# Kernel tuning notes

Hardware: AMD Instinct MI355X
Metric: run time of the kernel (lower is better)

The kernel has to match this reference:

```python
import jax, jax.numpy as jnp
import numpy as np

EPS = 1e-5  # torch InstanceNorm1d default


def _instance_norm_lastdim(t):
    # torch InstanceNorm1d applied to (b*h, n, d): normalizes over last axis d
    # per (b, h, n) with biased variance, no affine.
    mu = jnp.mean(t, axis=-1, keepdims=True)
    var = jnp.var(t, axis=-1, keepdims=True)
    return (t - mu) * jax.lax.rsqrt(var + EPS)


def setup_inputs() -> dict:
    key = jax.random.key(0)
    k1, k2, k3, k4 = jax.random.split(key, 4)
    b, n, dim = 4, 8192, 128
    heads, dim_head = 8, 64
    inner = heads * dim_head
    x = jax.random.normal(k1, (b, n, dim), dtype=jnp.float32)
    # nn.Linear(dim, inner*3, bias=False): weight (out, in); we store transposed (in, out)
    w_qkv = jax.random.normal(k2, (dim, inner * 3), dtype=jnp.float32) * (1.0 / np.sqrt(dim))
    w_out = jax.random.normal(k3, (inner, dim), dtype=jnp.float32) * (1.0 / np.sqrt(inner))
    b_out = jax.random.normal(k4, (dim,), dtype=jnp.float32) * 0.01
    return {"x": x, "w_qkv": w_qkv, "w_out": w_out, "b_out": b_out}


def reference(x, w_qkv, w_out, b_out):
    b, n, _ = x.shape
    heads, dim_head = 8, 64
    qkv = x @ w_qkv  # (b, n, 3*inner)
    q, k, v = jnp.split(qkv, 3, axis=-1)

    def to_heads(t):
        return t.reshape(b, n, heads, dim_head).transpose(0, 2, 1, 3)  # b h n d

    q, k, v = to_heads(q), to_heads(k), to_heads(v)
    # galerkin: norm k and v (InstanceNorm over dim_head axis)
    k = _instance_norm_lastdim(k)
    v = _instance_norm_lastdim(v)
    dots = jnp.einsum('bhnd,bhne->bhde', k, v)      # K^T V, small (d x d)
    out = jnp.einsum('bhnd,bhde->bhne', q, dots) * (1.0 / n)
    out = out.transpose(0, 2, 1, 3).reshape(b, n, heads * dim_head)
    return out @ w_out + b_out
```

## Files before the change

kernel.cpp:

```cpp
#include <hip/hip_runtime.h>

#define NN 8192
#define DIM 128

typedef short short8 __attribute__((ext_vector_type(8)));
typedef float f32x4 __attribute__((ext_vector_type(4)));

__device__ __forceinline__ unsigned short f2bf(float f) {
  unsigned int u = __float_as_uint(f);
  u = (u + 0x7FFFu + ((u >> 16) & 1u)) >> 16;
  return (unsigned short)u;
}
__device__ __forceinline__ unsigned int cvtpk(float a, float b) {
  unsigned int r;
  asm("v_cvt_pk_bf16_f32 %0, %1, %2" : "=v"(r) : "v"(a), "v"(b));
  return r;
}
__device__ __forceinline__ void gll16(const void* gsrc, void* ldst) {
  __builtin_amdgcn_global_load_lds(
      (const __attribute__((address_space(1))) unsigned int*)gsrc,
      (__attribute__((address_space(3))) unsigned int*)ldst, 16, 0, 0);
}
#define BAR_LGKM()                                          \
  do {                                                      \
    asm volatile("s_waitcnt lgkmcnt(0)" ::: "memory");      \
    __builtin_amdgcn_sched_barrier(0);                      \
    __builtin_amdgcn_s_barrier();                           \
    __builtin_amdgcn_sched_barrier(0);                      \
  } while (0)
#define BAR_VM()                                            \
  do {                                                      \
    asm volatile("s_waitcnt vmcnt(0)" ::: "memory");        \
    __builtin_amdgcn_sched_barrier(0);                      \
    __builtin_amdgcn_s_barrier();                           \
    __builtin_amdgcn_sched_barrier(0);                      \
  } while (0)

__global__ __launch_bounds__(256) void prep_kernel(const float* __restrict__ x,
                                                   const float* __restrict__ wqkv,
                                                   unsigned char* __restrict__ ximg,
                                                   unsigned char* __restrict__ wimg,
                                                   float* __restrict__ dots) {
  __shared__ __align__(16) unsigned char wb[32768];
  const int t = threadIdx.x;
  const int bx = blockIdx.x;
  if (bx < 1024) {
#pragma unroll
    for (int rep = 0; rep < 2; ++rep) {
      const int idx = bx * 512 + rep * 256 + t;
      const int bt = idx >> 10;
      const int o = (idx & 1023) << 4;
      const int r = o >> 8;
      const int q0 = o & 255;
      const int c0 = (q0 ^ ((r & 7) << 4)) >> 1;
      const float* src = x + ((size_t)(bt >> 7) * NN + (size_t)(bt & 127) * 64 + r) * DIM + c0;
      const float4 v0 = *(const float4*)src;
      const float4 v1 = *(const float4*)(src + 4);
      uint4 u;
      u.x = cvtpk(v0.x, v0.y);
      u.y = cvtpk(v0.z, v0.w);
      u.z = cvtpk(v1.x, v1.y);
      u.w = cvtpk(v1.z, v1.w);
      *(uint4*)(ximg + (size_t)idx * 16) = u;
    }
  } else if (bx < 1032) {
    const int h = bx - 1024;
    const int k = t >> 1;
    const int chalf = t & 1;
    const float* wp = wqkv + (size_t)k * 1536 + (chalf ? (1024 + h * 64) : (512 + h * 64));
    const float4* wp4 = (const float4*)wp;
    const int c0 = chalf * 64;
    float4 wv[16];
    float sum = 0.f;
#pragma unroll
    for (int jj = 0; jj < 16; ++jj) {
      wv[jj] = wp4[jj];
      sum += wv[jj].x + wv[jj].y + wv[jj].z + wv[jj].w;
    }
    const float mean = sum * (1.f / 64.f);
#pragma unroll
    for (int jj = 0; jj < 16; ++jj) {
      const int c = c0 + jj * 4;
      const unsigned int cx0 = (unsigned int)((c + 0) & 7) << 4;
      const unsigned int cx1 = (unsigned int)((c + 1) & 7) << 4;
      const unsigned int cx2 = (unsigned int)((c + 2) & 7) << 4;
      const unsigned int cx3 = (unsigned int)((c + 3) & 7) << 4;
      *(unsigned short*)(wb + (c + 0) * 256 + (((unsigned)(2 * k)) ^ cx0)) = f2bf(wv[jj].x - mean);
      *(unsigned short*)(wb + (c + 1) * 256 + (((unsigned)(2 * k)) ^ cx1)) = f2bf(wv[jj].y - mean);
      *(unsigned short*)(wb + (c + 2) * 256 + (((unsigned)(2 * k)) ^ cx2)) = f2bf(wv[jj].z - mean);
      *(unsigned short*)(wb + (c + 3) * 256 + (((unsigned)(2 * k)) ^ cx3)) = f2bf(wv[jj].w - mean);
    }
    __syncthreads();
    const uint4* s4 = (const uint4*)(wb + t * 128);
    uint4* d4 = (uint4*)(wimg + (size_t)h * 32768 + t * 128);
#pragma unroll
    for (int i = 0; i < 8; ++i) d4[i] = s4[i];
  } else {
    const int zb = bx - 1032;
    float4* dz = (float4*)dots + (size_t)zb * 4096 + t;
    const float4 z = make_float4(0.f, 0.f, 0.f, 0.f);
#pragma unroll
    for (int i = 0; i < 16; ++i) dz[i * 256] = z;
  }
}

__global__ __launch_bounds__(256) void kv_dots_v2(const unsigned char* __restrict__ ximg,
                                                  const unsigned char* __restrict__ wimg,
                                                  float* __restrict__ dots) {
  __shared__ __align__(16) unsigned char smem[81920];
  unsigned char* const XB0 = smem;
  unsigned char* const XB1 = smem + 16384;
  unsigned char* const WB = smem + 32768;
  unsigned char* const KT = smem + 65536;
  unsigned char* const VT = smem + 73728;

  const int t = threadIdx.x;
  const int bx = blockIdx.x;
  const int h = bx >> 7;
  const int p = bx & 127;
  const int b = p >> 5;
  const int chunk = p & 31;

  const int wave = t >> 6;
  const int lane = t & 63;
  const int lb = lane & 15;
  const int kg = lane >> 4;
  const unsigned int lxor = (unsigned int)(lb & 7) << 4;

  const unsigned char* wsrc = wimg + (size_t)h * 32768;
  const unsigned char* xsrc = ximg + (size_t)(b * 128 + chunk * 4) * 16384;

#pragma unroll
  for (int i = 0; i < 8; ++i)
    gll16(wsrc + (wave * 8 + i) * 1024 + lane * 16, WB + (wave * 8 + i) * 1024);
#pragma unroll
  for (int i = 0; i < 4; ++i)
    gll16(xsrc + (wave * 4 + i) * 1024 + lane * 16, XB0 + (wave * 4 + i) * 1024);

  f32x4 dacc[4];
#pragma unroll
  for (int nt = 0; nt < 4; ++nt) dacc[nt] = (f32x4)0.f;

  BAR_VM();

  unsigned char* XBc = XB0;
  unsigned char* XBn = XB1;
  const int arow = wave * 16 + lb;

  for (int tile = 0; tile < 4; ++tile) {
    if (tile < 3) {
#pragma unroll
      for (int i = 0; i < 4; ++i)
        gll16(xsrc + (size_t)(tile + 1) * 16384 + (wave * 4 + i) * 1024 + lane * 16,
              XBn + (wave * 4 + i) * 1024);
    }

    f32x4 acc[8];
#pragma unroll
    for (int ct = 0; ct < 8; ++ct) acc[ct] = (f32x4)0.f;
#pragma unroll
    for (int ks = 0; ks < 4; ++ks) {
      const unsigned int koff = (unsigned int)(ks * 64 + kg * 16);
      const short8 a = *(const short8*)(XBc + arow * 256 + (koff ^ lxor));
#pragma unroll
      for (int ct = 0; ct < 8; ++ct) {
        const short8 bf = *(const short8*)(WB + (ct * 16 + lb) * 256 + (koff ^ lxor));
        acc[ct] = __builtin_amdgcn_mfma_f32_16x16x32_bf16(a, bf, acc[ct], 0, 0, 0);
      }
    }

    float kscale[4];
#pragma unroll
    for (int e = 0; e < 4; ++e) {
      float sk = acc[0][e] * acc[0][e] + acc[1][e] * acc[1][e] +
                 acc[2][e] * acc[2][e] + acc[3][e] * acc[3][e];
      float sv = acc[4][e] * acc[4][e] + acc[5][e] * acc[5][e] +
                 acc[6][e] * acc[6][e] + acc[7][e] * acc[7][e];
      sk += __shfl_xor(sk, 1); sv += __shfl_xor(sv, 1);
      sk += __shfl_xor(sk, 2); sv += __shfl_xor(sv, 2);
      sk += __shfl_xor(sk, 4); sv += __shfl_xor(sv, 4);
      sk += __shfl_xor(sk, 8); sv += __shfl_xor(sv, 8);
      kscale[e] = rsqrtf(sk * (1.f / 64.f) + 1e-5f) * rsqrtf(sv * (1.f / 64.f) + 1e-5f);
    }

    {
      const unsigned int rb2 = (unsigned int)(32 * wave + kg * 8);
#pragma unroll
      for (int ct = 0; ct < 4; ++ct) {
        uint2 w;
        w.x = cvtpk(acc[ct][0] * kscale[0], acc[ct][1] * kscale[1]);
        w.y = cvtpk(acc[ct][2] * kscale[2], acc[ct][3] * kscale[3]);
        *(uint2*)(KT + (ct * 16 + lb) * 128 + (rb2 ^ lxor)) = w;
      }
#pragma unroll
      for (int ct = 4; ct < 8; ++ct) {
        uint2 w;
        w.x = cvtpk(acc[ct][0], acc[ct][1]);
        w.y = cvtpk(acc[ct][2], acc[ct][3]);
        *(uint2*)(VT + ((ct - 4) * 16 + lb) * 128 + (rb2 ^ lxor)) = w;
      }
    }
    BAR_LGKM();

#pragma unroll
    for (int ks2 = 0; ks2 < 2; ++ks2) {
      const unsigned int koff = (unsigned int)(ks2 * 64 + kg * 16);
      const short8 a = *(const short8*)(KT + (wave * 16 + lb) * 128 + (koff ^ lxor));
#pragma unroll
      for (int nt = 0; nt < 4; ++nt) {
        const short8 bf = *(const short8*)(VT + (nt * 16 + lb) * 128 + (koff ^ lxor));
        dacc[nt] = __builtin_amdgcn_mfma_f32_16x16x32_bf16(a, bf, dacc[nt], 0, 0, 0);
      }
    }
    BAR_VM();

    unsigned char* tmp = XBc; XBc = XBn; XBn = tmp;
  }

  float* dp = dots + (size_t)(b * 8 + h) * 4096;
#pragma unroll
  for (int nt = 0; nt < 4; ++nt) {
#pragma unroll
    for (int reg = 0; reg < 4; ++reg) {
      const int d = 16 * wave + kg * 4 + reg;
      const int e = nt * 16 + lb;
      atomicAdd(&dp[d * 64 + e], dacc[nt][reg]);
    }
  }
}

template <int TR>
__global__ __launch_bounds__(256) void tw_kernel(const float* __restrict__ wqkv,
                                                 const float* __restrict__ wout,
                                                 const float* __restrict__ dots,
                                                 float* __restrict__ part) {
  __shared__ __align__(16) float ds[64 * 66];
  __shared__ __align__(16) float wqT[64 * 36];
  __shared__ __align__(16) float Ts[32 * 66];
  __shared__ __align__(16) float wos[64 * 132];

  const int blk = blockIdx.x;
  const int bh = blk >> 2;
  const int cq = blk & 3;
  const int h = bh & 7;
  const int t = threadIdx.x;

  for (int i = t; i < 4096; i += 256)
    ds[(i >> 6) * 66 + (i & 63)] = dots[(size_t)bh * 4096 + i];

  for (int i = t; i < 2048; i += 256) {
    const int d = i >> 5;
    const int c = i & 31;
    wqT[d * 36 + c] = wqkv[(size_t)(cq * 32 + c) * 1536 + h * 64 + d];
  }

  for (int i = t; i < 2048; i += 256) {
    const int e = i >> 5;
    const int jj = (i & 31) * 4;
    *(float4*)&wos[e * 132 + jj] = *(const float4*)(wout + (size_t)(h * 64 + e) * 128 + jj);
  }
  __syncthreads();

  {
    const int c = t >> 3;
    const int e0 = (t & 7) * 8;
    float acc[8];
#pragma unroll
    for (int q = 0; q < 8; ++q) acc[q] = 0.f;
    for (int d = 0; d < 64; ++d) {
      const float wq = wqT[d * 36 + c];
      const float4 d0 = *(const float4*)&ds[d * 66 + e0];
      const float4 d1 = *(const float4*)&ds[d * 66 + e0 + 4];
      acc[0] += wq * d0.x; acc[1] += wq * d0.y; acc[2] += wq * d0.z; acc[3] += wq * d0.w;
      acc[4] += wq * d1.x; acc[5] += wq * d1.y; acc[6] += wq * d1.z; acc[7] += wq * d1.w;
    }
    *(float4*)&Ts[c * 66 + e0] = make_float4(acc[0], acc[1], acc[2], acc[3]);
    *(float4*)&Ts[c * 66 + e0 + 4] = make_float4(acc[4], acc[5], acc[6], acc[7]);
  }
  __syncthreads();

  {
    const int c = t >> 3;
    const int j0 = (t & 7) * 16;
    float acc[16];
#pragma unroll
    for (int q = 0; q < 16; ++q) acc[q] = 0.f;
    for (int e = 0; e < 64; ++e) {
      const float tv = Ts[c * 66 + e];
#pragma unroll
      for (int q = 0; q < 16; q += 4) {
        const float4 wv = *(const float4*)&wos[e * 132 + j0 + q];
        acc[q + 0] += tv * wv.x;
        acc[q + 1] += tv * wv.y;
        acc[q + 2] += tv * wv.z;
        acc[q + 3] += tv * wv.w;
      }
    }
    if (TR) {
      float* pp = part + (size_t)bh * 16384;
      const int cc = cq * 32 + c;
#pragma unroll
      for (int q = 0; q < 16; ++q) pp[(j0 + q) * 128 + cc] = acc[q];
    } else {
      float* pp = part + (size_t)bh * 16384 + (size_t)(cq * 32 + c) * 128 + j0;
#pragma unroll
      for (int q = 0; q < 16; q += 4)
        *(float4*)&pp[q] = make_float4(acc[q], acc[q + 1], acc[q + 2], acc[q + 3]);
    }
  }
}

__global__ __launch_bounds__(256) void bigw_reduce_v2(const float* __restrict__ part,
                                                      unsigned char* __restrict__ bigwimg) {
  const int idx = blockIdx.x * 256 + threadIdx.x;
  const int b = idx >> 11;
  const int o = (idx & 2047) << 4;
  const int j = o >> 8;
  const int q0 = o & 255;
  const int c0 = (q0 ^ ((j & 7) << 4)) >> 1;
  float s[8];
#pragma unroll
  for (int i = 0; i < 8; ++i) s[i] = 0.f;
  const float* pb = part + (size_t)b * 8 * 16384 + j * 128 + c0;
#pragma unroll
  for (int hh = 0; hh < 8; ++hh) {
    const float4 p0 = *(const float4*)(pb + hh * 16384);
    const float4 p1 = *(const float4*)(pb + hh * 16384 + 4);
    s[0] += p0.x; s[1] += p0.y; s[2] += p0.z; s[3] += p0.w;
    s[4] += p1.x; s[5] += p1.y; s[6] += p1.z; s[7] += p1.w;
  }
  const float inv_n = 1.f / (float)NN;
  uint4 u;
  u.x = cvtpk(s[0] * inv_n, s[1] * inv_n);
  u.y = cvtpk(s[2] * inv_n, s[3] * inv_n);
  u.z = cvtpk(s[4] * inv_n, s[5] * inv_n);
  u.w = cvtpk(s[6] * inv_n, s[7] * inv_n);
  *(uint4*)(bigwimg + (size_t)idx * 16) = u;
}

__global__ __launch_bounds__(256) void out_v2(const unsigned char* __restrict__ ximg,
                                              const unsigned char* __restrict__ bigwimg,
                                              const float* __restrict__ bout,
                                              float* __restrict__ out) {
  __shared__ __align__(16) unsigned char smem[49152];
  unsigned char* const XB = smem;
  unsigned char* const WJ = smem + 16384;

  const int t = threadIdx.x;
  const int bx = blockIdx.x;
  const int b = bx >> 7;
  const int tile = bx & 127;

  const int wave = t >> 6;
  const int lane = t & 63;
  const int lb = lane & 15;
  const int kg = lane >> 4;
  const unsigned int lxor = (unsigned int)(lb & 7) << 4;

  const unsigned char* wsrc = bigwimg + (size_t)b * 32768;
  const unsigned char* xsrc = ximg + (size_t)(b * 128 + tile) * 16384;

#pragma unroll
  for (int i = 0; i < 8; ++i)
    gll16(wsrc + (wave * 8 + i) * 1024 + lane * 16, WJ + (wave * 8 + i) * 1024);
#pragma unroll
  for (int i = 0; i < 4; ++i)
    gll16(xsrc + (wave * 4 + i) * 1024 + lane * 16, XB + (wave * 4 + i) * 1024);

  float bias[8];
#pragma unroll
  for (int ct = 0; ct < 8; ++ct) bias[ct] = bout[ct * 16 + lb];

  BAR_VM();

  f32x4 acc[8];
#pragma unroll
  for (int ct = 0; ct < 8; ++ct) acc[ct] = (f32x4)0.f;
  const int arow = wave * 16 + lb;
#pragma unroll
  for (int ks = 0; ks < 4; ++ks) {
    const unsigned int koff = (unsigned int)(ks * 64 + kg * 16);
    const short8 a = *(const short8*)(XB + arow * 256 + (koff ^ lxor));
#pragma unroll
    for (int ct = 0; ct < 8; ++ct) {
      const short8 bf = *(const short8*)(WJ + (ct * 16 + lb) * 256 + (koff ^ lxor));
      acc[ct] = __builtin_amdgcn_mfma_f32_16x16x32_bf16(a, bf, acc[ct], 0, 0, 0);
    }
  }

  float* op = out + (size_t)(b * NN + tile * 64 + 16 * wave + kg * 4) * DIM;
#pragma unroll
  for (int ct = 0; ct < 8; ++ct) {
#pragma unroll
    for (int reg = 0; reg < 4; ++reg) {
      op[reg * DIM + ct * 16 + lb] = acc[ct][reg] + bias[ct];
    }
  }
}

__global__ __launch_bounds__(256) void zero_dots_fb(float* __restrict__ dots) {
  float4* dz = (float4*)dots + (size_t)blockIdx.x * 4096 + threadIdx.x;
  const float4 z = make_float4(0.f, 0.f, 0.f, 0.f);
#pragma unroll
  for (int i = 0; i < 16; ++i) dz[i * 256] = z;
}

__global__ __launch_bounds__(256) void kv_dots_fb(const float* __restrict__ x,
                                                  const float* __restrict__ wqkv,
                                                  float* __restrict__ dots) {
  __shared__ __align__(16) unsigned char smem[49152];
  unsigned char* const XB = smem;
  unsigned char* const KT = smem;
  unsigned char* const VT = smem + 8192;
  unsigned char* const WB = smem + 16384;

  const int t = threadIdx.x;
  const int bx = blockIdx.x;
  const int h = bx >> 7;
  const int p = bx & 127;
  const int b = p >> 5;
  const int chunk = p & 31;
  const int row0 = chunk * 256;

  const int wave = t >> 6;
  const int lane = t & 63;
  const int lb = lane & 15;
  const int kg = lane >> 4;
  const unsigned int lxor = (unsigned int)(lb & 7) << 4;

  {
    const int k = t >> 1;
    const int chalf = t & 1;
    const float* wp = wqkv + (size_t)k * 1536 + (chalf ? (1024 + h * 64) : (512 + h * 64));
    const float4* wp4 = (const float4*)wp;
    const int c0 = chalf * 64;
    float4 wv[16];
    float sum = 0.f;
#pragma unroll
    for (int jj = 0; jj < 16; ++jj) {
      wv[jj] = wp4[jj];
      sum += wv[jj].x + wv[jj].y + wv[jj].z + wv[jj].w;
    }
    const float mean = sum * (1.f / 64.f);
#pragma unroll
    for (int jj = 0; jj < 16; ++jj) {
      const int c = c0 + jj * 4;
      const unsigned int cx0 = (unsigned int)((c + 0) & 7) << 4;
      const unsigned int cx1 = (unsigned int)((c + 1) & 7) << 4;
      const unsigned int cx2 = (unsigned int)((c + 2) & 7) << 4;
      const unsigned int cx3 = (unsigned int)((c + 3) & 7) << 4;
      *(unsigned short*)(WB + (c + 0) * 256 + (((unsigned)(2 * k)) ^ cx0)) = f2bf(wv[jj].x - mean);
      *(unsigned short*)(WB + (c + 1) * 256 + (((unsigned)(2 * k)) ^ cx1)) = f2bf(wv[jj].y - mean);
      *(unsigned short*)(WB + (c + 2) * 256 + (((unsigned)(2 * k)) ^ cx2)) = f2bf(wv[jj].z - mean);
      *(unsigned short*)(WB + (c + 3) * 256 + (((unsigned)(2 * k)) ^ cx3)) = f2bf(wv[jj].w - mean);
    }
  }

  f32x4 dacc[4];
#pragma unroll
  for (int nt = 0; nt < 4; ++nt) dacc[nt] = (f32x4)0.f;

  __syncthreads();

  for (int tile = 0; tile < 4; ++tile) {
    const int rowbase = row0 + tile * 64;
    __syncthreads();
    {
      const int r = t >> 2;
      const int cb = (t & 3) * 32;
      const float4* gp4 = (const float4*)(x + (size_t)(b * NN + rowbase + r) * DIM + cb);
      const unsigned int rxor = (unsigned int)(r & 7) << 4;
#pragma unroll
      for (int jj = 0; jj < 4; ++jj) {
        const float4 v0 = gp4[2 * jj];
        const float4 v1 = gp4[2 * jj + 1];
        uint4 u;
        u.x = cvtpk(v0.x, v0.y);
        u.y = cvtpk(v0.z, v0.w);
        u.z = cvtpk(v1.x, v1.y);
        u.w = cvtpk(v1.z, v1.w);
        *(uint4*)(XB + r * 256 + (((unsigned)(2 * cb + 16 * jj)) ^ rxor)) = u;
      }
    }
    __syncthreads();

    f32x4 acc[8];
#pragma unroll
    for (int ct = 0; ct < 8; ++ct) acc[ct] = (f32x4)0.f;
    const int arow = wave * 16 + lb;
#pragma unroll
    for (int ks = 0; ks < 4; ++ks) {
      const unsigned int koff = (unsigned int)(ks * 64 + kg * 16);
      const short8 a = *(const short8*)(XB + arow * 256 + (koff ^ lxor));
#pragma unroll
      for (int ct = 0; ct < 8; ++ct) {
        const short8 bf = *(const short8*)(WB + (ct * 16 + lb) * 256 + (koff ^ lxor));
        acc[ct] = __builtin_amdgcn_mfma_f32_16x16x32_bf16(a, bf, acc[ct], 0, 0, 0);
      }
    }

    float kscale[4];
#pragma unroll
    for (int e = 0; e < 4; ++e) {
      float sk = acc[0][e] * acc[0][e] + acc[1][e] * acc[1][e] +
                 acc[2][e] * acc[2][e] + acc[3][e] * acc[3][e];
      float sv = acc[4][e] * acc[4][e] + acc[5][e] * acc[5][e] +
                 acc[6][e] * acc[6][e] + acc[7][e] * acc[7][e];
      sk += __shfl_xor(sk, 1); sv += __shfl_xor(sv, 1);
      sk += __shfl_xor(sk, 2); sv += __shfl_xor(sv, 2);
      sk += __shfl_xor(sk, 4); sv += __shfl_xor(sv, 4);
      sk += __shfl_xor(sk, 8); sv += __shfl_xor(sv, 8);
      kscale[e] = rsqrtf(sk * (1.f / 64.f) + 1e-5f) * rsqrtf(sv * (1.f / 64.f) + 1e-5f);
    }

    __syncthreads();
    {
      const unsigned int rb2 = (unsigned int)(32 * wave + kg * 8);
#pragma unroll
      for (int ct = 0; ct < 4; ++ct) {
        uint2 w;
        w.x = cvtpk(acc[ct][0] * kscale[0], acc[ct][1] * kscale[1]);
        w.y = cvtpk(acc[ct][2] * kscale[2], acc[ct][3] * kscale[3]);
        *(uint2*)(KT + (ct * 16 + lb) * 128 + (rb2 ^ lxor)) = w;
      }
#pragma unroll
      for (int ct = 4; ct < 8; ++ct) {
        uint2 w;
        w.x = cvtpk(acc[ct][0], acc[ct][1]);
        w.y = cvtpk(acc[ct][2], acc[ct][3]);
        *(uint2*)(VT + ((ct - 4) * 16 + lb) * 128 + (rb2 ^ lxor)) = w;
      }
    }
    __syncthreads();

#pragma unroll
    for (int ks2 = 0; ks2 < 2; ++ks2) {
      const unsigned int koff = (unsigned int)(ks2 * 64 + kg * 16);
      const short8 a = *(const short8*)(KT + (wave * 16 + lb) * 128 + (koff ^ lxor));
#pragma unroll
      for (int nt = 0; nt < 4; ++nt) {
        const short8 bf = *(const short8*)(VT + (nt * 16 + lb) * 128 + (koff ^ lxor));
        dacc[nt] = __builtin_amdgcn_mfma_f32_16x16x32_bf16(a, bf, dacc[nt], 0, 0, 0);
      }
    }
  }

  float* dp = dots + (size_t)(b * 8 + h) * 4096;
#pragma unroll
  for (int nt = 0; nt < 4; ++nt) {
#pragma unroll
    for (int reg = 0; reg < 4; ++reg) {
      const int d = 16 * wave + kg * 4 + reg;
      const int e = nt * 16 + lb;
      atomicAdd(&dp[d * 64 + e], dacc[nt][reg]);
    }
  }
}

__global__ __launch_bounds__(256) void bigw_reduce_fb(const float* __restrict__ part,
                                                      float* __restrict__ bigw) {
  const int i = blockIdx.x * 256 + threadIdx.x;
  const int b = i >> 14;
  const int cj = i & 16383;
  const float* pp = part + (size_t)b * 8 * 16384 + cj;
  float s = 0.f;
#pragma unroll
  for (int h = 0; h < 8; ++h) s += pp[h * 16384];
  bigw[i] = s * (1.f / (float)NN);
}

__global__ __launch_bounds__(256) void out_fb(const float* __restrict__ x,
                                              const float* __restrict__ bigw,
                                              const float* __restrict__ bout,
                                              float* __restrict__ out) {
  __shared__ __align__(16) unsigned char smem[49152];
  unsigned char* const XB = smem;
  unsigned char* const WB = smem + 16384;

  const int t = threadIdx.x;
  const int bx = blockIdx.x;
  const int b = bx >> 7;
  const int rowbase = (bx & 127) * 64;

  const int wave = t >> 6;
  const int lane = t & 63;
  const int lb = lane & 15;
  const int kg = lane >> 4;
  const unsigned int lxor = (unsigned int)(lb & 7) << 4;

  {
    const int c = t >> 1;
    const int jhalf = t & 1;
    const float4* wp4 = (const float4*)(bigw + (size_t)b * 16384 + (size_t)c * 128 + jhalf * 64);
    const int j0 = jhalf * 64;
#pragma unroll
    for (int q = 0; q < 16; ++q) {
      const float4 v = wp4[q];
      const int j = j0 + q * 4;
      const unsigned int jx0 = (unsigned int)((j + 0) & 7) << 4;
      const unsigned int jx1 = (unsigned int)((j + 1) & 7) << 4;
      const unsigned int jx2 = (unsigned int)((j + 2) & 7) << 4;
      const unsigned int jx3 = (unsigned int)((j + 3) & 7) << 4;
      *(unsigned short*)(WB + (j + 0) * 256 + (((unsigned)(2 * c)) ^ jx0)) = f2bf(v.x);
      *(unsigned short*)(WB + (j + 1) * 256 + (((unsigned)(2 * c)) ^ jx1)) = f2bf(v.y);
      *(unsigned short*)(WB + (j + 2) * 256 + (((unsigned)(2 * c)) ^ jx2)) = f2bf(v.z);
      *(unsigned short*)(WB + (j + 3) * 256 + (((unsigned)(2 * c)) ^ jx3)) = f2bf(v.w);
    }
  }

  float bias[8];
#pragma unroll
  for (int ct = 0; ct < 8; ++ct) bias[ct] = bout[ct * 16 + lb];

  {
    const int r = t >> 2;
    const int cb = (t & 3) * 32;
    const float4* gp4 = (const float4*)(x + (size_t)(b * NN + rowbase + r) * DIM + cb);
    const unsigned int rxor = (unsigned int)(r & 7) << 4;
#pragma unroll
    for (int jj = 0; jj < 4; ++jj) {
      const float4 v0 = gp4[2 * jj];
      const float4 v1 = gp4[2 * jj + 1];
      uint4 u;
      u.x = cvtpk(v0.x, v0.y);
      u.y = cvtpk(v0.z, v0.w);
      u.z = cvtpk(v1.x, v1.y);
      u.w = cvtpk(v1.z, v1.w);
      *(uint4*)(XB + r * 256 + (((unsigned)(2 * cb + 16 * jj)) ^ rxor)) = u;
    }
  }
  __syncthreads();

  f32x4 acc[8];
#pragma unroll
  for (int ct = 0; ct < 8; ++ct) acc[ct] = (f32x4)0.f;
  const int arow = wave * 16 + lb;
#pragma unroll
  for (int ks = 0; ks < 4; ++ks) {
    const unsigned int koff = (unsigned int)(ks * 64 + kg * 16);
    const short8 a = *(const short8*)(XB + arow * 256 + (koff ^ lxor));
#pragma unroll
    for (int ct = 0; ct < 8; ++ct) {
      const short8 bf = *(const short8*)(WB + (ct * 16 + lb) * 256 + (koff ^ lxor));
      acc[ct] = __builtin_amdgcn_mfma_f32_16x16x32_bf16(a, bf, acc[ct], 0, 0, 0);
    }
  }

  float* op = out + (size_t)(b * NN + rowbase + 16 * wave + kg * 4) * DIM;
#pragma unroll
  for (int ct = 0; ct < 8; ++ct) {
#pragma unroll
    for (int reg = 0; reg < 4; ++reg) {
      op[reg * DIM + ct * 16 + lb] = acc[ct][reg] + bias[ct];
    }
  }
}

extern "C" void kernel_launch(void* const* d_in, const int* in_sizes, int n_in,
                              void* d_out, int out_size, void* d_ws, size_t ws_size,
                              hipStream_t stream) {
  (void)in_sizes; (void)n_in; (void)out_size;
  const float* x = (const float*)d_in[0];
  const float* wqkv = (const float*)d_in[1];
  const float* wout = (const float*)d_in[2];
  const float* bout = (const float*)d_in[3];
  float* out = (float*)d_out;

  const size_t NEED = 8388608ull + 262144ull + 131072ull + 524288ull + 2097152ull;
  if (ws_size >= NEED) {
    unsigned char* ximg = (unsigned char*)d_ws;
    unsigned char* wimg = ximg + 8388608;
    unsigned char* bigwimg = wimg + 262144;
    float* dots = (float*)(bigwimg + 131072);
    float* part = dots + 131072;

    hipLaunchKernelGGL(prep_kernel, dim3(1040), dim3(256), 0, stream, x, wqkv, ximg, wimg, dots);
    hipLaunchKernelGGL(kv_dots_v2, dim3(1024), dim3(256), 0, stream, ximg, wimg, dots);
    hipLaunchKernelGGL((tw_kernel<1>), dim3(128), dim3(256), 0, stream, wqkv, wout, dots, part);
    hipLaunchKernelGGL(bigw_reduce_v2, dim3(32), dim3(256), 0, stream, part, bigwimg);
    hipLaunchKernelGGL(out_v2, dim3(512), dim3(256), 0, stream, ximg, bigwimg, bout, out);
  } else {
    float* dots = (float*)d_ws;
    float* part = dots + 131072;
    float* bigw = part + 524288;
    hipLaunchKernelGGL(zero_dots_fb, dim3(8), dim3(256), 0, stream, dots);
    hipLaunchKernelGGL(kv_dots_fb, dim3(1024), dim3(256), 0, stream, x, wqkv, dots);
    hipLaunchKernelGGL((tw_kernel<0>), dim3(128), dim3(256), 0, stream, wqkv, wout, dots, part);
    hipLaunchKernelGGL(bigw_reduce_fb, dim3(256), dim3(256), 0, stream, part, bigw);
    hipLaunchKernelGGL(out_fb, dim3(512), dim3(256), 0, stream, x, bigw, bout, out);
  }
}
```

Measured before the change: 70.56 us.

## Restructure kv_dots to 512 threads with all row tiles loaded at once

Replaces the 4-iteration double-buffered loop over 64-row X tiles in the K/V projection plus KᵀV kernel with a single pass using 8 waves. Each wave loads and projects its own 32 rows at once, writes normalized K and V transposed into a per-wave LDS slab, and then each wave accumulates one 16x32 slice of the 64x64 dots across all 8 slabs. This removes the serial tile loop and its per-tile barriers, and halves the number of atomics per thread. In exchange it uses 96KB of LDS per block, which limits occupancy, and drops the overlap of loads with compute.

```diff
diff --git a/kernel.cpp b/kernel.cpp
--- a/kernel.cpp
+++ b/kernel.cpp
@@ -104,15 +104,11 @@
   }
 }
 
-__global__ __launch_bounds__(256) void kv_dots_v2(const unsigned char* __restrict__ ximg,
+__global__ __launch_bounds__(512) void kv_dots_v3(const unsigned char* __restrict__ ximg,
                                                   const unsigned char* __restrict__ wimg,
                                                   float* __restrict__ dots) {
-  __shared__ __align__(16) unsigned char smem[81920];
-  unsigned char* const XB0 = smem;
-  unsigned char* const XB1 = smem + 16384;
-  unsigned char* const WB = smem + 32768;
-  unsigned char* const KT = smem + 65536;
-  unsigned char* const VT = smem + 73728;
+  __shared__ __align__(16) unsigned char smem[98304];
+  unsigned char* const WB = smem;
 
   const int t = threadIdx.x;
   const int bx = blockIdx.x;
@@ -126,105 +122,106 @@
   const int lb = lane & 15;
   const int kg = lane >> 4;
   const unsigned int lxor = (unsigned int)(lb & 7) << 4;
-
-  const unsigned char* wsrc = wimg + (size_t)h * 32768;
-  const unsigned char* xsrc = ximg + (size_t)(b * 128 + chunk * 4) * 16384;
-
-#pragma unroll
-  for (int i = 0; i < 8; ++i)
-    gll16(wsrc + (wave * 8 + i) * 1024 + lane * 16, WB + (wave * 8 + i) * 1024);
-#pragma unroll
-  for (int i = 0; i < 4; ++i)
-    gll16(xsrc + (wave * 4 + i) * 1024 + lane * 16, XB0 + (wave * 4 + i) * 1024);
-
-  f32x4 dacc[4];
-#pragma unroll
-  for (int nt = 0; nt < 4; ++nt) dacc[nt] = (f32x4)0.f;
-
+  const unsigned int rxor2 = (unsigned int)(lb & 3) << 4;
+
+  unsigned char* const PW = smem + 32768 + wave * 8192;
+
+  {
+    const unsigned char* wsrc = wimg + (size_t)h * 32768;
+#pragma unroll
+    for (int i = 0; i < 4; ++i)
+      gll16(wsrc + (wave * 4 + i) * 1024 + lane * 16, WB + (wave * 4 + i) * 1024);
+    const unsigned char* xsrc = ximg +
+        (size_t)(b * 128 + chunk * 4 + (wave >> 1)) * 16384 + (size_t)(wave & 1) * 8192;
+#pragma unroll
+    for (int i = 0; i < 8; ++i)
+      gll16(xsrc + i * 1024 + lane * 16, PW + i * 1024);
+  }
   BAR_VM();
 
-  unsigned char* XBc = XB0;
-  unsigned char* XBn = XB1;
-  const int arow = wave * 16 + lb;
-
-  for (int tile = 0; tile < 4; ++tile) {
-    if (tile < 3) {
-#pragma unroll
-      for (int i = 0; i < 4; ++i)
-        gll16(xsrc + (size_t)(tile + 1) * 16384 + (wave * 4 + i) * 1024 + lane * 16,
-              XBn + (wave * 4 + i) * 1024);
-    }
-
-    f32x4 acc[8];
-#pragma unroll
-    for (int ct = 0; ct < 8; ++ct) acc[ct] = (f32x4)0.f;
-#pragma unroll
-    for (int ks = 0; ks < 4; ++ks) {
-      const unsigned int koff = (unsigned int)(ks * 64 + kg * 16);
-      const short8 a = *(const short8*)(XBc + arow * 256 + (koff ^ lxor));
+  f32x4 acc[2][8];
+#pragma unroll
+  for (int rg = 0; rg < 2; ++rg)
+#pragma unroll
+    for (int ct = 0; ct < 8; ++ct) acc[rg][ct] = (f32x4)0.f;
+
+#pragma unroll
+  for (int ks = 0; ks < 4; ++ks) {
+    const unsigned int koff = (unsigned int)(ks * 64 + kg * 16);
+#pragma unroll
+    for (int rg = 0; rg < 2; ++rg) {
+      const short8 a = *(const short8*)(PW + (rg * 16 + lb) * 256 + (koff ^ lxor));
 #pragma unroll
       for (int ct = 0; ct < 8; ++ct) {
         const short8 bf = *(const short8*)(WB + (ct * 16 + lb) * 256 + (koff ^ lxor));
-        acc[ct] = __builtin_amdgcn_mfma_f32_16x16x32_bf16(a, bf, acc[ct], 0, 0, 0);
+        acc[rg][ct] = __builtin_amdgcn_mfma_f32_16x16x32_bf16(a, bf, acc[rg][ct], 0, 0, 0);
       }
     }
-
-    float kscale[4];
+  }
+
+  float ks[2][4];
+#pragma unroll
+  for (int rg = 0; rg < 2; ++rg) {
 #pragma unroll
     for (int e = 0; e < 4; ++e) {
-      float sk = acc[0][e] * acc[0][e] + acc[1][e] * acc[1][e] +
-                 acc[2][e] * acc[2][e] + acc[3][e] * acc[3][e];
-      float sv = acc[4][e] * acc[4][e] + acc[5][e] * acc[5][e] +
-                 acc[6][e] * acc[6][e] + acc[7][e] * acc[7][e];
+      float sk = acc[rg][0][e] * acc[rg][0][e] + acc[rg][1][e] * acc[rg][1][e] +
+                 acc[rg][2][e] * acc[rg][2][e] + acc[rg][3][e] * acc[rg][3][e];
+      float sv = acc[rg][4][e] * acc[rg][4][e] + acc[rg][5][e] * acc[rg][5][e] +
+                 acc[rg][6][e] * acc[rg][6][e] + acc[rg][7][e] * acc[rg][7][e];
       sk += __shfl_xor(sk, 1); sv += __shfl_xor(sv, 1);
       sk += __shfl_xor(sk, 2); sv += __shfl_xor(sv, 2);
       sk += __shfl_xor(sk, 4); sv += __shfl_xor(sv, 4);
       sk += __shfl_xor(sk, 8); sv += __shfl_xor(sv, 8);
-      kscale[e] = rsqrtf(sk * (1.f / 64.f) + 1e-5f) * rsqrtf(sv * (1.f / 64.f) + 1e-5f);
-    }
-
-    {
-      const unsigned int rb2 = (unsigned int)(32 * wave + kg * 8);
-#pragma unroll
-      for (int ct = 0; ct < 4; ++ct) {
-        uint2 w;
-        w.x = cvtpk(acc[ct][0] * kscale[0], acc[ct][1] * kscale[1]);
-        w.y = cvtpk(acc[ct][2] * kscale[2], acc[ct][3] * kscale[3]);
-        *(uint2*)(KT + (ct * 16 + lb) * 128 + (rb2 ^ lxor)) = w;
-      }
-#pragma unroll
-      for (int ct = 4; ct < 8; ++ct) {
-        uint2 w;
-        w.x = cvtpk(acc[ct][0], acc[ct][1]);
-        w.y = cvtpk(acc[ct][2], acc[ct][3]);
-        *(uint2*)(VT + ((ct - 4) * 16 + lb) * 128 + (rb2 ^ lxor)) = w;
-      }
-    }
-    BAR_LGKM();
-
-#pragma unroll
-    for (int ks2 = 0; ks2 < 2; ++ks2) {
-      const unsigned int koff = (unsigned int)(ks2 * 64 + kg * 16);
-      const short8 a = *(const short8*)(KT + (wave * 16 + lb) * 128 + (koff ^ lxor));
-#pragma unroll
-      for (int nt = 0; nt < 4; ++nt) {
-        const short8 bf = *(const short8*)(VT + (nt * 16 + lb) * 128 + (koff ^ lxor));
-        dacc[nt] = __builtin_amdgcn_mfma_f32_16x16x32_bf16(a, bf, dacc[nt], 0, 0, 0);
-      }
-    }
-    BAR_VM();
-
-    unsigned char* tmp = XBc; XBc = XBn; XBn = tmp;
+      ks[rg][e] = rsqrtf(sk * (1.f / 64.f) + 1e-5f) * rsqrtf(sv * (1.f / 64.f) + 1e-5f);
+    }
+  }
+  __builtin_amdgcn_sched_barrier(0);
+
+#pragma unroll
+  for (int rg = 0; rg < 2; ++rg) {
+    const unsigned int rb = ((unsigned int)(rg * 32 + kg * 8)) ^ rxor2;
+#pragma unroll
+    for (int ct = 0; ct < 4; ++ct) {
+      uint2 w;
+      w.x = cvtpk(acc[rg][ct][0] * ks[rg][0], acc[rg][ct][1] * ks[rg][1]);
+      w.y = cvtpk(acc[rg][ct][2] * ks[rg][2], acc[rg][ct][3] * ks[rg][3]);
+      *(uint2*)(PW + (ct * 16 + lb) * 64 + rb) = w;
+    }
+#pragma unroll
+    for (int ct = 4; ct < 8; ++ct) {
+      uint2 w;
+      w.x = cvtpk(acc[rg][ct][0], acc[rg][ct][1]);
+      w.y = cvtpk(acc[rg][ct][2], acc[rg][ct][3]);
+      *(uint2*)(PW + 4096 + (ct - 4) * 1024 + lb * 64 + rb) = w;
+    }
+  }
+  BAR_LGKM();
+
+  const int dt = wave >> 1;
+  const int ntb = (wave & 1) * 2;
+  f32x4 dacc[2];
+  dacc[0] = (f32x4)0.f;
+  dacc[1] = (f32x4)0.f;
+  const unsigned int soff = ((unsigned int)(kg * 16)) ^ rxor2;
+#pragma unroll
+  for (int s = 0; s < 8; ++s) {
+    const unsigned char* P = smem + 32768 + s * 8192;
+    const short8 a = *(const short8*)(P + (dt * 16 + lb) * 64 + soff);
+#pragma unroll
+    for (int j = 0; j < 2; ++j) {
+      const short8 bf = *(const short8*)(P + 4096 + ((ntb + j) * 16 + lb) * 64 + soff);
+      dacc[j] = __builtin_amdgcn_mfma_f32_16x16x32_bf16(a, bf, dacc[j], 0, 0, 0);
+    }
   }
 
   float* dp = dots + (size_t)(b * 8 + h) * 4096;
 #pragma unroll
-  for (int nt = 0; nt < 4; ++nt) {
+  for (int j = 0; j < 2; ++j) {
 #pragma unroll
     for (int reg = 0; reg < 4; ++reg) {
-      const int d = 16 * wave + kg * 4 + reg;
-      const int e = nt * 16 + lb;
-      atomicAdd(&dp[d * 64 + e], dacc[nt][reg]);
+      const int d = dt * 16 + kg * 4 + reg;
+      const int e = (ntb + j) * 16 + lb;
+      atomicAdd(&dp[d * 64 + e], dacc[j][reg]);
     }
   }
 }
@@ -675,7 +672,7 @@
     float* part = dots + 131072;
 
     hipLaunchKernelGGL(prep_kernel, dim3(1040), dim3(256), 0, stream, x, wqkv, ximg, wimg, dots);
-    hipLaunchKernelGGL(kv_dots_v2, dim3(1024), dim3(256), 0, stream, ximg, wimg, dots);
+    hipLaunchKernelGGL(kv_dots_v3, dim3(1024), dim3(512), 0, stream, ximg, wimg, dots);
     hipLaunchKernelGGL((tw_kernel<1>), dim3(128), dim3(256), 0, stream, wqkv, wout, dots, part);
     hipLaunchKernelGGL(bigw_reduce_v2, dim3(32), dim3(256), 0, stream, part, bigwimg);
     hipLaunchKernelGGL(out_v2, dim3(512), dim3(256), 0, stream, ximg, bigwimg, bout, out);
```

Result: no change. 71.88 us (+1.9%).

## Restructure kv_dots to load X fragments into registers and split K/V across waves

Applied to the files above, without the earlier changes.

The kv_dots kernel stops staging X tiles in shared memory and instead loads each wave's MFMA A fragments directly from global memory into registers, prefetching the next tile. Waves are regrouped so pairs handle K and V columns separately over 32-row subtiles, which halves the per-wave accumulator set. LDS drops from 80KB to 40KB and launch bounds request 4 blocks per CU, aiming at higher occupancy. In exchange there are twice as many tile iterations, each with two barriers, and global loads are no longer coalesced through LDS.

```diff
diff --git a/kernel.cpp b/kernel.cpp
--- a/kernel.cpp
+++ b/kernel.cpp
@@ -104,15 +104,13 @@
   }
 }
 
-__global__ __launch_bounds__(256) void kv_dots_v2(const unsigned char* __restrict__ ximg,
-                                                  const unsigned char* __restrict__ wimg,
-                                                  float* __restrict__ dots) {
-  __shared__ __align__(16) unsigned char smem[81920];
-  unsigned char* const XB0 = smem;
-  unsigned char* const XB1 = smem + 16384;
-  unsigned char* const WB = smem + 32768;
-  unsigned char* const KT = smem + 65536;
-  unsigned char* const VT = smem + 73728;
+__global__ __launch_bounds__(256, 4) void kv_dots_v4(const unsigned char* __restrict__ ximg,
+                                                     const unsigned char* __restrict__ wimg,
+                                                     float* __restrict__ dots) {
+  __shared__ __align__(16) unsigned char smem[40960];
+  unsigned char* const WB = smem;
+  unsigned char* const KT = smem + 32768;
+  unsigned char* const VT = smem + 36864;
 
   const int t = threadIdx.x;
   const int bx = blockIdx.x;
@@ -125,106 +123,101 @@
   const int lane = t & 63;
   const int lb = lane & 15;
   const int kg = lane >> 4;
+  const int g = wave & 1;
+  const int ch = wave >> 1;
   const unsigned int lxor = (unsigned int)(lb & 7) << 4;
+  const unsigned int rxor = (unsigned int)(lb & 3) << 4;
 
   const unsigned char* wsrc = wimg + (size_t)h * 32768;
   const unsigned char* xsrc = ximg + (size_t)(b * 128 + chunk * 4) * 16384;
 
 #pragma unroll
   for (int i = 0; i < 8; ++i)
-    gll16(wsrc + (wave * 8 + i) * 1024 + lane * 16, WB + (wave * 8 + i) * 1024);
-#pragma unroll
-  for (int i = 0; i < 4; ++i)
-    gll16(xsrc + (wave * 4 + i) * 1024 + lane * 16, XB0 + (wave * 4 + i) * 1024);
+    gll16(wsrc + (i * 4 + wave) * 1024 + lane * 16, WB + (i * 4 + wave) * 1024);
+
+  const int rrow = 16 * g + lb;
+  short8 xf[4];
+#pragma unroll
+  for (int ks = 0; ks < 4; ++ks)
+    xf[ks] = *(const short8*)(xsrc + rrow * 256 + (((unsigned)(ks * 64 + kg * 16)) ^ lxor));
 
   f32x4 dacc[4];
 #pragma unroll
-  for (int nt = 0; nt < 4; ++nt) dacc[nt] = (f32x4)0.f;
+  for (int et = 0; et < 4; ++et) dacc[et] = (f32x4)0.f;
 
   BAR_VM();
 
-  unsigned char* XBc = XB0;
-  unsigned char* XBn = XB1;
-  const int arow = wave * 16 + lb;
-
-  for (int tile = 0; tile < 4; ++tile) {
-    if (tile < 3) {
-#pragma unroll
-      for (int i = 0; i < 4; ++i)
-        gll16(xsrc + (size_t)(tile + 1) * 16384 + (wave * 4 + i) * 1024 + lane * 16,
-              XBn + (wave * 4 + i) * 1024);
-    }
-
-    f32x4 acc[8];
-#pragma unroll
-    for (int ct = 0; ct < 8; ++ct) acc[ct] = (f32x4)0.f;
+  unsigned char* const MYT = ch ? VT : KT;
+
+  for (int tile = 0; tile < 8; ++tile) {
+    short8 xn[4];
+    if (tile < 7) {
+      const unsigned char* tb = xsrc + (size_t)((tile + 1) >> 1) * 16384 + (size_t)((tile + 1) & 1) * 8192;
+#pragma unroll
+      for (int ks = 0; ks < 4; ++ks)
+        xn[ks] = *(const short8*)(tb + rrow * 256 + (((unsigned)(ks * 64 + kg * 16)) ^ lxor));
+    }
+
+    f32x4 acc[4];
+#pragma unroll
+    for (int ct = 0; ct < 4; ++ct) acc[ct] = (f32x4)0.f;
 #pragma unroll
     for (int ks = 0; ks < 4; ++ks) {
-      const unsigned int koff = (unsigned int)(ks * 64 + kg * 16);
-      const short8 a = *(const short8*)(XBc + arow * 256 + (koff ^ lxor));
-#pragma unroll
-      for (int ct = 0; ct < 8; ++ct) {
-        const short8 bf = *(const short8*)(WB + (ct * 16 + lb) * 256 + (koff ^ lxor));
-        acc[ct] = __builtin_amdgcn_mfma_f32_16x16x32_bf16(a, bf, acc[ct], 0, 0, 0);
-      }
-    }
-
-    float kscale[4];
+      const unsigned int koff = ((unsigned)(ks * 64 + kg * 16)) ^ lxor;
+#pragma unroll
+      for (int ct = 0; ct < 4; ++ct) {
+        const short8 bf = *(const short8*)(WB + (ch * 64 + ct * 16 + lb) * 256 + koff);
+        acc[ct] = __builtin_amdgcn_mfma_f32_16x16x32_bf16(xf[ks], bf, acc[ct], 0, 0, 0);
+      }
+    }
+
+    float sc[4];
 #pragma unroll
     for (int e = 0; e < 4; ++e) {
-      float sk = acc[0][e] * acc[0][e] + acc[1][e] * acc[1][e] +
-                 acc[2][e] * acc[2][e] + acc[3][e] * acc[3][e];
-      float sv = acc[4][e] * acc[4][e] + acc[5][e] * acc[5][e] +
-                 acc[6][e] * acc[6][e] + acc[7][e] * acc[7][e];
-      sk += __shfl_xor(sk, 1); sv += __shfl_xor(sv, 1);
-      sk += __shfl_xor(sk, 2); sv += __shfl_xor(sv, 2);
-      sk += __shfl_xor(sk, 4); sv += __shfl_xor(sv, 4);
-      sk += __shfl_xor(sk, 8); sv += __shfl_xor(sv, 8);
-      kscale[e] = rsqrtf(sk * (1.f / 64.f) + 1e-5f) * rsqrtf(sv * (1.f / 64.f) + 1e-5f);
+      float s = acc[0][e] * acc[0][e] + acc[1][e] * acc[1][e] +
+                acc[2][e] * acc[2][e] + acc[3][e] * acc[3][e];
+      s += __shfl_xor(s, 1);
+      s += __shfl_xor(s, 2);
+      s += __shfl_xor(s, 4);
+      s += __shfl_xor(s, 8);
+      sc[e] = rsqrtf(s * (1.f / 64.f) + 1e-5f);
     }
 
     {
-      const unsigned int rb2 = (unsigned int)(32 * wave + kg * 8);
+      const unsigned int rb = ((unsigned)(g * 32 + kg * 8)) ^ rxor;
 #pragma unroll
       for (int ct = 0; ct < 4; ++ct) {
-        uint2 w;
-        w.x = cvtpk(acc[ct][0] * kscale[0], acc[ct][1] * kscale[1]);
-        w.y = cvtpk(acc[ct][2] * kscale[2], acc[ct][3] * kscale[3]);
-        *(uint2*)(KT + (ct * 16 + lb) * 128 + (rb2 ^ lxor)) = w;
-      }
-#pragma unroll
-      for (int ct = 4; ct < 8; ++ct) {
-        uint2 w;
-        w.x = cvtpk(acc[ct][0], acc[ct][1]);
-        w.y = cvtpk(acc[ct][2], acc[ct][3]);
-        *(uint2*)(VT + ((ct - 4) * 16 + lb) * 128 + (rb2 ^ lxor)) = w;
+        uint2 w2;
+        w2.x = cvtpk(acc[ct][0] * sc[0], acc[ct][1] * sc[1]);
+        w2.y = cvtpk(acc[ct][2] * sc[2], acc[ct][3] * sc[3]);
+        *(uint2*)(MYT + (ct * 16 + lb) * 64 + rb) = w2;
       }
     }
     BAR_LGKM();
 
-#pragma unroll
-    for (int ks2 = 0; ks2 < 2; ++ks2) {
-      const unsigned int koff = (unsigned int)(ks2 * 64 + kg * 16);
-      const short8 a = *(const short8*)(KT + (wave * 16 + lb) * 128 + (koff ^ lxor));
-#pragma unroll
-      for (int nt = 0; nt < 4; ++nt) {
-        const short8 bf = *(const short8*)(VT + (nt * 16 + lb) * 128 + (koff ^ lxor));
-        dacc[nt] = __builtin_amdgcn_mfma_f32_16x16x32_bf16(a, bf, dacc[nt], 0, 0, 0);
-      }
-    }
-    BAR_VM();
-
-    unsigned char* tmp = XBc; XBc = XBn; XBn = tmp;
+    {
+      const unsigned int soff = ((unsigned)(kg * 16)) ^ rxor;
+      const short8 a = *(const short8*)(KT + (wave * 16 + lb) * 64 + soff);
+#pragma unroll
+      for (int et = 0; et < 4; ++et) {
+        const short8 bf = *(const short8*)(VT + (et * 16 + lb) * 64 + soff);
+        dacc[et] = __builtin_amdgcn_mfma_f32_16x16x32_bf16(a, bf, dacc[et], 0, 0, 0);
+      }
+    }
+    BAR_LGKM();
+
+#pragma unroll
+    for (int ks = 0; ks < 4; ++ks) xf[ks] = xn[ks];
   }
 
   float* dp = dots + (size_t)(b * 8 + h) * 4096;
 #pragma unroll
-  for (int nt = 0; nt < 4; ++nt) {
+  for (int et = 0; et < 4; ++et) {
 #pragma unroll
     for (int reg = 0; reg < 4; ++reg) {
-      const int d = 16 * wave + kg * 4 + reg;
-      const int e = nt * 16 + lb;
-      atomicAdd(&dp[d * 64 + e], dacc[nt][reg]);
+      const int d = wave * 16 + kg * 4 + reg;
+      const int e = et * 16 + lb;
+      atomicAdd(&dp[d * 64 + e], dacc[et][reg]);
     }
   }
 }
@@ -675,7 +668,7 @@
     float* part = dots + 131072;
 
     hipLaunchKernelGGL(prep_kernel, dim3(1040), dim3(256), 0, stream, x, wqkv, ximg, wimg, dots);
-    hipLaunchKernelGGL(kv_dots_v2, dim3(1024), dim3(256), 0, stream, ximg, wimg, dots);
+    hipLaunchKernelGGL(kv_dots_v4, dim3(1024), dim3(256), 0, stream, ximg, wimg, dots);
     hipLaunchKernelGGL((tw_kernel<1>), dim3(128), dim3(256), 0, stream, wqkv, wout, dots, part);
     hipLaunchKernelGGL(bigw_reduce_v2, dim3(32), dim3(256), 0, stream, part, bigwimg);
     hipLaunchKernelGGL(out_v2, dim3(512), dim3(256), 0, stream, ximg, bigwimg, bout, out);
```

Measured after the change: 65.87 us, median of 2. -6.7%, faster.
